# Kernel optimization log

Measured on AMD Instinct MI355X. Metric: run time of the kernel, lower is better.

Reference implementation:

```python
import jax, jax.numpy as jnp
import numpy as np

N, T, IN_F, H, C_OUT, R = 50000, 128, 6, 32, 32, 16
NUM_EDGES, N_INC = 2000, 150000


def setup_inputs() -> dict:
    key = jax.random.key(0)
    ks = jax.random.split(key, 16)
    s = 0.1  # param scale
    return {
        "price_input": jax.random.normal(ks[0], (N, T, IN_F), jnp.float32),
        "concept": jax.random.normal(ks[1], (N_INC,), jnp.float32),
        "W_ih": jax.random.normal(ks[2], (3 * H, IN_F), jnp.float32) * s,
        "W_hh": jax.random.normal(ks[3], (3 * H, H), jnp.float32) * s,
        "b_ih": jax.random.normal(ks[4], (3 * H,), jnp.float32) * s,
        "b_hh": jax.random.normal(ks[5], (3 * H,), jnp.float32) * s,
        "W1": jax.random.normal(ks[6], (C_OUT, H), jnp.float32) * s,
        "b1": jax.random.normal(ks[7], (C_OUT,), jnp.float32) * s,
        "W2": jax.random.normal(ks[8], (H, C_OUT), jnp.float32) * s,
        "b2": jax.random.normal(ks[9], (H,), jnp.float32) * s,
        "Wl": jax.random.normal(ks[10], (R, H), jnp.float32) * s,
        "bl": jax.random.normal(ks[11], (R,), jnp.float32) * s,
        "node_idx": jax.random.randint(ks[12], (N_INC,), 0, N, dtype=jnp.int32),
        "edge_idx": jax.random.randint(ks[13], (N_INC,), 0, NUM_EDGES, dtype=jnp.int32),
    }


def gru_last_hidden(x, W_ih, W_hh, b_ih, b_hh):
    # x: [N, T, IN_F] -> final hidden state [N, H] (PyTorch GRU, gate order r,z,n)
    gi_all = jnp.einsum('nti,gi->tng', x, W_ih) + b_ih  # [T, N, 3H]
    h0 = jnp.zeros((x.shape[0], W_hh.shape[1]), x.dtype)

    def step(h, gi):
        gh = h @ W_hh.T + b_hh
        ir, iz, i_n = jnp.split(gi, 3, axis=-1)
        hr, hz, h_n = jnp.split(gh, 3, axis=-1)
        r = jax.nn.sigmoid(ir + hr)
        z = jax.nn.sigmoid(iz + hz)
        n = jnp.tanh(i_n + r * h_n)
        return (1.0 - z) * n + z * h, None

    hT, _ = jax.lax.scan(step, h0, gi_all)
    return hT


def hypergraph_conv(x, W, b, node_idx, edge_idx, num_nodes, num_edges):
    # PyG HypergraphConv, use_attention=False, hyperedge_weight=1:
    # out = D^{-1} H B^{-1} H^T (X W^T) + b
    xw = x @ W.T  # [N, F_out]
    ones = jnp.ones(node_idx.shape[0], x.dtype)
    B = jax.ops.segment_sum(ones, edge_idx, num_segments=num_edges)
    Binv = jnp.where(B > 0, 1.0 / B, 0.0)
    edge_feat = jax.ops.segment_sum(xw[node_idx], edge_idx, num_segments=num_edges)
    edge_feat = edge_feat * Binv[:, None]
    D = jax.ops.segment_sum(ones, node_idx, num_segments=num_nodes)
    Dinv = jnp.where(D > 0, 1.0 / D, 0.0)
    out = jax.ops.segment_sum(edge_feat[edge_idx], node_idx, num_segments=num_nodes)
    return out * Dinv[:, None] + b


def reference(price_input, concept, W_ih, W_hh, b_ih, b_hh, W1, b1, W2, b2, Wl, bl, node_idx, edge_idx):
    # concept is only consumed on the PreAttn path (disabled here), kept for signature parity.
    num_nodes = price_input.shape[0]
    output = gru_last_hidden(price_input, W_ih, W_hh, b_ih, b_hh)  # query[0] -> [N, c_in]
    output = jax.nn.leaky_relu(output, 0.01)
    x = jax.nn.leaky_relu(
        hypergraph_conv(output, W1, b1, node_idx, edge_idx, num_nodes, NUM_EDGES), 0.2)
    x = jax.nn.leaky_relu(
        hypergraph_conv(x, W2, b2, node_idx, edge_idx, num_nodes, NUM_EDGES), 0.2)
    return jax.nn.leaky_relu(x @ Wl.T + bl, 0.01)  # [N, len(rr_num)]
```

## Files before the change

### kernel.cpp

```cpp
#include <hip/hip_runtime.h>
#include <hip/hip_bf16.h>
#include <cstdint>

#define NN 50000
#define TT 128
#define INF 6
#define HH 32
#define NE 2000
#define NI 150000
#define RR 16

typedef __attribute__((ext_vector_type(4)))  float f32x4;
typedef __attribute__((ext_vector_type(16))) float f32x16;
typedef __attribute__((ext_vector_type(8)))  short short8;

__device__ __forceinline__ float lrelu(float x, float s){ return x > 0.f ? x : s*x; }

__device__ __forceinline__ unsigned pk2(float a, float b){
  union { __hip_bfloat162 h; unsigned u; } t;
  t.h = __float22bfloat162_rn(make_float2(a, b));
  return t.u;
}
__device__ __forceinline__ void pkhl(float a, float b, unsigned &hi, unsigned &lo){
  hi = pk2(a, b);
  float ha = __uint_as_float(hi << 16);
  float hb = __uint_as_float(hi & 0xFFFF0000u);
  lo = pk2(a - ha, b - hb);
}
__device__ __forceinline__ unsigned pksplit(float x){
  unsigned h = pk2(x, 0.f) & 0xFFFFu;
  float hf = __uint_as_float(h << 16);
  unsigned l = pk2(x - hf, 0.f) & 0xFFFFu;
  return h | (l << 16);
}
__device__ __forceinline__ short8 mk8(unsigned a, unsigned b, unsigned c, unsigned d){
  union { unsigned u[4]; short8 v; } t;
  t.u[0]=a; t.u[1]=b; t.u[2]=c; t.u[3]=d;
  return t.v;
}
#define MFMA32 __builtin_amdgcn_mfma_f32_32x32x16_bf16

__global__ __launch_bounds__(64,2) void gru_mfma(
    const float* __restrict__ price,
    const float* __restrict__ W_ih, const float* __restrict__ W_hh,
    const float* __restrict__ b_ih, const float* __restrict__ b_hh,
    const float* __restrict__ W1,
    float* __restrict__ xw, float* __restrict__ eaccZ)
{
  __shared__ __align__(16) unsigned xs[2][2048];

  const int lane = threadIdx.x;
  const int a    = lane & 31;
  const int hb   = lane >> 5;
  const int n0   = blockIdx.x*32;

  { int gt = blockIdx.x*64 + lane; if (gt < NE*HH) eaccZ[gt] = 0.f; }

  for (int idx = lane; idx < 512; idx += 64){
    int bsel = idx >> 8, rem = idx & 255;
    int nd = rem >> 3, t7 = rem & 7;
    int swz = (nd&7)<<2;
    xs[bsel][nd*64 + ((t7*8+6) ^ swz)] = 0x3F803F80u;
    xs[bsel][nd*64 + ((t7*8+7) ^ swz)] = 0u;
  }

  short8 AxA[3], Ahh[3][2], Ahl[3][2];
#pragma unroll
  for (int T=0; T<3; T++){
    const int gr = T*32 + a;
    const float sc = (T<2) ? -1.44269504f : 2.88539008f;
    const float* vi = W_ih + gr*INF;
    const float w0=vi[0]*sc, w1=vi[1]*sc, w2=vi[2]*sc, w3=vi[3]*sc, w4=vi[4]*sc, w5=vi[5]*sc;
    const float bias = (b_ih[gr] + ((T<2) ? b_hh[gr] : 0.f)) * sc;
    if (hb==0) AxA[T] = mk8(pk2(w0,w1), pk2(w2,w3), pk2(w4,w5), pk2(w0,w1));
    else       AxA[T] = mk8(pk2(w2,w3), pk2(w4,w5), pksplit(bias), 0u);
#pragma unroll
    for (int m=0; m<2; m++){
      const float* wp = W_hh + gr*HH + m*16 + hb*8;
      float4 wa = *(const float4*)(wp);
      float4 wb = *(const float4*)(wp+4);
      wa.x*=sc; wa.y*=sc; wa.z*=sc; wa.w*=sc;
      wb.x*=sc; wb.y*=sc; wb.z*=sc; wb.w*=sc;
      unsigned h0,l0,h1,l1,h2,l2,h3,l3;
      pkhl(wa.x,wa.y,h0,l0); pkhl(wa.z,wa.w,h1,l1);
      pkhl(wb.x,wb.y,h2,l2); pkhl(wb.z,wb.w,h3,l3);
      Ahh[T][m] = mk8(h0,h1,h2,h3);
      Ahl[T][m] = mk8(l0,l1,l2,l3);
    }
  }
  f32x16 BHN;
#pragma unroll
  for (int r=0; r<16; r++){
    int row = (r&3) + 8*(r>>2) + 4*hb;
    BHN[r] = b_hh[2*HH + row] * 2.88539008f;
  }
  const f32x16 Z16 = {0.f,0.f,0.f,0.f,0.f,0.f,0.f,0.f,0.f,0.f,0.f,0.f,0.f,0.f,0.f,0.f};

  float h[16];
#pragma unroll
  for (int r=0;r<16;r++) h[r]=0.f;
  short8 Bh1 = mk8(0,0,0,0), Bh2 = mk8(0,0,0,0);

  float4 ld[6];
#define PREFETCH(C) { \
  _Pragma("unroll") \
  for (int q=0;q<6;q++){ \
    int id=q*64+lane, a2=id/12, off=id%12; \
    int na=n0+a2; if (na>NN-1) na=NN-1; \
    ld[q] = *(const float4*)(price + (size_t)na*(TT*INF) + (C)*48 + off*4); \
  } }
#define STAGE(BUF) { \
  _Pragma("unroll") \
  for (int q=0;q<6;q++){ \
    int id=q*64+lane, a2=id/12, off=id%12; \
    int swz=(a2&7)<<2; unsigned* row=(BUF)+a2*64; \
    _Pragma("unroll") \
    for (int p=0;p<2;p++){ \
      float e0 = p? ld[q].z : ld[q].x; \
      float e1 = p? ld[q].w : ld[q].y; \
      int b = off*4 + p*2; int ttl = b/6; int ii = b - ttl*6; \
      unsigned hi_, lo_; pkhl(e0, e1, hi_, lo_); \
      row[(ttl*8 + (ii>>1)) ^ swz]     = hi_; \
      row[(ttl*8 + 3 + (ii>>1)) ^ swz] = lo_; \
    } } }

  PREFETCH(0); STAGE(&xs[0][0]);

  const int roff = (hb<<2) ^ ((a&7)<<2);

#pragma unroll 1
  for (int c=0;c<16;c++){
    if (c<15) PREFETCH(c+1);
    const unsigned* cell = &xs[c&1][a*64];
    unsigned* sb = &xs[(c&1)^1][0];
#pragma unroll 1
    for (int tt=0; tt<8; tt++){
      union{uint4 u; short8 s;} cv;
      cv.u = *(const uint4*)(cell + ((tt*8) ^ roff));
      f32x16 aR  = MFMA32(AxA[0], cv.s, Z16, 0,0,0);
      f32x16 aZ  = MFMA32(AxA[1], cv.s, Z16, 0,0,0);
      f32x16 aNX = MFMA32(AxA[2], cv.s, Z16, 0,0,0);
      f32x16 aNH = MFMA32(Ahh[2][0], Bh1, BHN, 0,0,0);
      aR = MFMA32(Ahh[0][0], Bh1, aR, 0,0,0); aR = MFMA32(Ahh[0][1], Bh2, aR, 0,0,0);
      aR = MFMA32(Ahl[0][0], Bh1, aR, 0,0,0); aR = MFMA32(Ahl[0][1], Bh2, aR, 0,0,0);
      aZ = MFMA32(Ahh[1][0], Bh1, aZ, 0,0,0); aZ = MFMA32(Ahh[1][1], Bh2, aZ, 0,0,0);
      aZ = MFMA32(Ahl[1][0], Bh1, aZ, 0,0,0); aZ = MFMA32(Ahl[1][1], Bh2, aZ, 0,0,0);
      aNH= MFMA32(Ahh[2][1], Bh2, aNH,0,0,0);
      aNH= MFMA32(Ahl[2][0], Bh1, aNH,0,0,0); aNH= MFMA32(Ahl[2][1], Bh2, aNH,0,0,0);
#define GUPD(hvar, AR, AZ, ANX, ANH) { \
      float er = __builtin_amdgcn_exp2f(AR); \
      float rr = __builtin_amdgcn_rcpf(1.f + er); \
      float p  = (ANX) + rr*(ANH); \
      float ez = __builtin_amdgcn_exp2f(AZ); \
      float et = __builtin_amdgcn_exp2f(p); \
      float etp = et + 1.f, etm = et - 1.f; \
      float num = hvar*etp + ez*etm; \
      float den = (1.f + ez) * etp; \
      hvar = num * __builtin_amdgcn_rcpf(den); }
#pragma unroll
      for (int r=0;r<16;r++) GUPD(h[r], aR[r], aZ[r], aNX[r], aNH[r]);
      unsigned c0=pk2(h[0],h[1]),  c1=pk2(h[2],h[3]),  c2=pk2(h[4],h[5]),  c3=pk2(h[6],h[7]);
      unsigned c4=pk2(h[8],h[9]),  c5=pk2(h[10],h[11]), c6=pk2(h[12],h[13]), c7=pk2(h[14],h[15]);
      unsigned p0=__shfl_xor(c0,32,64), p1=__shfl_xor(c1,32,64);
      unsigned p2=__shfl_xor(c2,32,64), p3=__shfl_xor(c3,32,64);
      unsigned p4=__shfl_xor(c4,32,64), p5=__shfl_xor(c5,32,64);
      unsigned p6=__shfl_xor(c6,32,64), p7=__shfl_xor(c7,32,64);
      unsigned v0 = hb? p2 : c0, v1 = hb? p3 : c1, v2 = hb? c2 : p0, v3 = hb? c3 : p1;
      unsigned w0 = hb? p6 : c4, w1 = hb? p7 : c5, w2 = hb? c6 : p4, w3 = hb? c7 : p5;
      Bh1 = mk8(v0,v1,v2,v3);
      Bh2 = mk8(w0,w1,w2,w3);
    }
    if (c<15) STAGE(sb);
  }

  float* ldsF = (float*)&xs[0][0];
#pragma unroll
  for (int r=0;r<16;r++){
    int row = (r&3) + 8*(r>>2) + 4*hb;
    ldsF[a*33 + row] = lrelu(h[r], 0.01f);
  }
  float b1v[8], b2v[8];
#pragma unroll
  for (int e=0;e<8;e++){
    b1v[e] = ldsF[a*33 + hb*8 + e];
    b2v[e] = ldsF[a*33 + 16 + hb*8 + e];
  }
  unsigned q0,s0,q1,s1,q2,s2,q3,s3;
  pkhl(b1v[0],b1v[1],q0,s0); pkhl(b1v[2],b1v[3],q1,s1);
  pkhl(b1v[4],b1v[5],q2,s2); pkhl(b1v[6],b1v[7],q3,s3);
  short8 Brh1 = mk8(q0,q1,q2,q3), Brl1 = mk8(s0,s1,s2,s3);
  pkhl(b2v[0],b2v[1],q0,s0); pkhl(b2v[2],b2v[3],q1,s1);
  pkhl(b2v[4],b2v[5],q2,s2); pkhl(b2v[6],b2v[7],q3,s3);
  short8 Brh2 = mk8(q0,q1,q2,q3), Brl2 = mk8(s0,s1,s2,s3);
  short8 W1h[2], W1l[2];
#pragma unroll
  for (int m=0;m<2;m++){
    const float* wp = W1 + a*HH + m*16 + hb*8;
    float4 wa = *(const float4*)(wp);
    float4 wb = *(const float4*)(wp+4);
    unsigned h0,l0,h1,l1,h2,l2,h3,l3;
    pkhl(wa.x,wa.y,h0,l0); pkhl(wa.z,wa.w,h1,l1);
    pkhl(wb.x,wb.y,h2,l2); pkhl(wb.z,wb.w,h3,l3);
    W1h[m] = mk8(h0,h1,h2,h3);
    W1l[m] = mk8(l0,l1,l2,l3);
  }
  f32x16 o = MFMA32(W1h[0], Brh1, Z16, 0,0,0);
  o = MFMA32(W1h[1], Brh2, o, 0,0,0);
  o = MFMA32(W1h[0], Brl1, o, 0,0,0);
  o = MFMA32(W1h[1], Brl2, o, 0,0,0);
  o = MFMA32(W1l[0], Brh1, o, 0,0,0);
  o = MFMA32(W1l[1], Brh2, o, 0,0,0);
#pragma unroll
  for (int r=0;r<16;r++){
    int row = (r&3) + 8*(r>>2) + 4*hb;
    ldsF[a*33 + row] = o[r];
  }
  {
    int nn = lane>>1, f0 = (lane&1)*16;
    if (n0 + nn < NN){
#pragma unroll
      for (int q=0;q<4;q++){
        float4 v;
        v.x = ldsF[nn*33 + f0 + q*4 + 0];
        v.y = ldsF[nn*33 + f0 + q*4 + 1];
        v.z = ldsF[nn*33 + f0 + q*4 + 2];
        v.w = ldsF[nn*33 + f0 + q*4 + 3];
        *(float4*)(xw + (size_t)(n0+nn)*HH + f0 + q*4) = v;
      }
    }
  }
}

template<bool COUNT>
__global__ __launch_bounds__(256) void scat_e(const float* __restrict__ xw, const int* __restrict__ nidx,
                                              const int* __restrict__ eidx, float* __restrict__ eacc,
                                              float* __restrict__ degD, float* __restrict__ degB){
  int idx = blockIdx.x*256 + threadIdx.x;
  int i = idx >> 5, f = idx & 31;
  int nd = nidx[i], e = eidx[i];
  if (COUNT && f == 0){
    atomicAdd(&degD[nd], 1.f);
    atomicAdd(&degB[e], 1.f);
  }
  atomicAdd(&eacc[(size_t)e*HH + f], xw[(size_t)nd*HH + f]);
}
template __global__ void scat_e<true>(const float*, const int*, const int*, float*, float*, float*);
template __global__ void scat_e<false>(const float*, const int*, const int*, float*, float*, float*);

__global__ __launch_bounds__(256) void scat_n(const float* __restrict__ eacc, const float* __restrict__ degB,
                                              const int* __restrict__ nidx, const int* __restrict__ eidx,
                                              float* __restrict__ nacc){
  int idx = blockIdx.x*256 + threadIdx.x;
  int i = idx >> 5, f = idx & 31;
  int nd = nidx[i], e = eidx[i];
  float b = degB[e];
  float binv = b > 0.f ? 1.f/b : 0.f;
  atomicAdd(&nacc[(size_t)nd*HH + f], eacc[(size_t)e*HH + f]*binv);
}

__global__ __launch_bounds__(256) void finmm(float* __restrict__ nacc, const float* __restrict__ degD,
                                             const float* __restrict__ bias, const float* __restrict__ W,
                                             float* __restrict__ Y, float* __restrict__ eacc){
  __shared__ float sWt[HH*HH];
  __shared__ float sX[8*HH];
  int tid = threadIdx.x;
  if (blockIdx.x < 250) eacc[blockIdx.x*256 + tid] = 0.f;
  int f0 = tid>>5, k = tid&31;
#pragma unroll
  for (int q=0;q<4;q++) sWt[k*HH + (q*8+f0)] = W[(q*8+f0)*HH + k];
  size_t base = (size_t)blockIdx.x*8*HH;
  int n = blockIdx.x*8 + (tid>>5);
  float d = degD[n];
  float dinv = d > 0.f ? 1.f/d : 0.f;
  sX[tid] = lrelu(nacc[base + tid]*dinv + bias[tid&31], 0.2f);
  nacc[base + tid] = 0.f;
  __syncthreads();
  float a = 0.f;
#pragma unroll
  for (int kk=0;kk<HH;kk++) a += sX[(tid>>5)*HH+kk]*sWt[kk*HH+(tid&31)];
  Y[base + tid] = a;
}

__global__ __launch_bounds__(256) void fin_final(const float* __restrict__ nacc, const float* __restrict__ degD,
                                                 const float* __restrict__ b2, const float* __restrict__ Wl,
                                                 const float* __restrict__ bl, float* __restrict__ out){
  __shared__ float sWl[HH*RR];
  __shared__ float sX[8*HH];
  int tid = threadIdx.x;
#pragma unroll
  for (int q=0;q<2;q++){
    int idx = q*256 + tid;
    int r = idx >> 5, kk = idx & 31;
    sWl[kk*RR + r] = Wl[idx];
  }
  size_t base = (size_t)blockIdx.x*8*HH;
  int n = blockIdx.x*8 + (tid>>5);
  float d = degD[n];
  float dinv = d > 0.f ? 1.f/d : 0.f;
  sX[tid] = lrelu(nacc[base + tid]*dinv + b2[tid&31], 0.2f);
  __syncthreads();
  int ln = tid>>5, r = tid&31;
  if (r < RR){
    float a = bl[r];
#pragma unroll
    for (int kk=0;kk<HH;kk++) a += sX[ln*HH+kk]*sWl[kk*RR+r];
    out[(size_t)(blockIdx.x*8+ln)*RR + r] = lrelu(a, 0.01f);
  }
}

extern "C" void kernel_launch(void* const* d_in, const int* in_sizes, int n_in,
                              void* d_out, int out_size, void* d_ws, size_t ws_size,
                              hipStream_t stream){
  const float* price = (const float*)d_in[0];
  const float* W_ih = (const float*)d_in[2];
  const float* W_hh = (const float*)d_in[3];
  const float* b_ih = (const float*)d_in[4];
  const float* b_hh = (const float*)d_in[5];
  const float* W1   = (const float*)d_in[6];
  const float* b1   = (const float*)d_in[7];
  const float* W2   = (const float*)d_in[8];
  const float* b2   = (const float*)d_in[9];
  const float* Wl   = (const float*)d_in[10];
  const float* bl   = (const float*)d_in[11];
  const int* nidx   = (const int*)d_in[12];
  const int* eidx   = (const int*)d_in[13];
  float* out = (float*)d_out;

  float* ws   = (float*)d_ws;
  float* xw   = ws;
  float* nacc = ws + 1600000;
  float* degD = ws + 3200000;
  float* degB = ws + 3250000;
  float* eacc = out;

  hipMemsetAsync(nacc, 0, (1600000+52000)*sizeof(float), stream);

  gru_mfma<<<1563, 64, 0, stream>>>(price, W_ih, W_hh, b_ih, b_hh, W1, xw, eacc);

  scat_e<true><<<18750, 256, 0, stream>>>(xw, nidx, eidx, eacc, degD, degB);
  scat_n<<<18750, 256, 0, stream>>>(eacc, degB, nidx, eidx, nacc);
  finmm<<<6250, 256, 0, stream>>>(nacc, degD, b1, W2, xw, eacc);

  scat_e<false><<<18750, 256, 0, stream>>>(xw, nidx, eidx, eacc, degD, degB);
  scat_n<<<18750, 256, 0, stream>>>(eacc, degB, nidx, eidx, nacc);
  fin_final<<<6250, 256, 0, stream>>>(nacc, degD, b2, Wl, bl, out);
}
```

Baseline: 347.3 us.

## Switch GRU recurrence to 16x16x32 MFMA with 16 nodes per wave

The GRU kernel is rebuilt around 16x16x32 bf16 MFMAs. Each wave now handles 16 nodes instead of 32, and the launch doubles to 3125 blocks with launch_bounds raised to 3 waves per SIMD. The hidden state feeds back directly as the B operand, which drops the cross-half shuffles of the old 32x32 layout and halves the LDS staging buffer. The aim is to shorten the serial per-step latency chain and raise occupancy. The cost is that two lane groups in the input MFMAs carry only zero padding, and the recurrent bf16 hi/lo split now covers only the weights, since the hidden state is packed as plain bf16.

```diff
diff --git a/kernel.cpp b/kernel.cpp
--- a/kernel.cpp
+++ b/kernel.cpp
@@ -11,7 +11,6 @@
 #define RR 16
 
 typedef __attribute__((ext_vector_type(4)))  float f32x4;
-typedef __attribute__((ext_vector_type(16))) float f32x16;
 typedef __attribute__((ext_vector_type(8)))  short short8;
 
 __device__ __forceinline__ float lrelu(float x, float s){ return x > 0.f ? x : s*x; }
@@ -38,80 +37,75 @@
   t.u[0]=a; t.u[1]=b; t.u[2]=c; t.u[3]=d;
   return t.v;
 }
-#define MFMA32 __builtin_amdgcn_mfma_f32_32x32x16_bf16
-
-__global__ __launch_bounds__(64,2) void gru_mfma(
+#define MFMA16 __builtin_amdgcn_mfma_f32_16x16x32_bf16
+
+__global__ __launch_bounds__(64,3) void gru_mfma(
     const float* __restrict__ price,
     const float* __restrict__ W_ih, const float* __restrict__ W_hh,
     const float* __restrict__ b_ih, const float* __restrict__ b_hh,
     const float* __restrict__ W1,
     float* __restrict__ xw, float* __restrict__ eaccZ)
 {
-  __shared__ __align__(16) unsigned xs[2][2048];
+  __shared__ __align__(16) unsigned xs[2][1024];
 
   const int lane = threadIdx.x;
-  const int a    = lane & 31;
-  const int hb   = lane >> 5;
-  const int n0   = blockIdx.x*32;
+  const int c    = lane & 15;
+  const int g    = lane >> 4;
+  const int n0   = blockIdx.x*16;
 
   { int gt = blockIdx.x*64 + lane; if (gt < NE*HH) eaccZ[gt] = 0.f; }
 
-  for (int idx = lane; idx < 512; idx += 64){
-    int bsel = idx >> 8, rem = idx & 255;
+  for (int idx = lane; idx < 256; idx += 64){
+    int bsel = idx >> 7, rem = idx & 127;
     int nd = rem >> 3, t7 = rem & 7;
     int swz = (nd&7)<<2;
     xs[bsel][nd*64 + ((t7*8+6) ^ swz)] = 0x3F803F80u;
     xs[bsel][nd*64 + ((t7*8+7) ^ swz)] = 0u;
   }
 
-  short8 AxA[3], Ahh[3][2], Ahl[3][2];
-#pragma unroll
-  for (int T=0; T<3; T++){
-    const int gr = T*32 + a;
-    const float sc = (T<2) ? -1.44269504f : 2.88539008f;
+  short8 Ax[6], Ahh[6], Ahl[6];
+  f32x4 BHN[2];
+#pragma unroll
+  for (int q=0;q<6;q++){
+    const int gr = q*16 + c;
+    const float sc = (q<4) ? -1.44269504f : 2.88539008f;
     const float* vi = W_ih + gr*INF;
     const float w0=vi[0]*sc, w1=vi[1]*sc, w2=vi[2]*sc, w3=vi[3]*sc, w4=vi[4]*sc, w5=vi[5]*sc;
-    const float bias = (b_ih[gr] + ((T<2) ? b_hh[gr] : 0.f)) * sc;
-    if (hb==0) AxA[T] = mk8(pk2(w0,w1), pk2(w2,w3), pk2(w4,w5), pk2(w0,w1));
-    else       AxA[T] = mk8(pk2(w2,w3), pk2(w4,w5), pksplit(bias), 0u);
-#pragma unroll
-    for (int m=0; m<2; m++){
-      const float* wp = W_hh + gr*HH + m*16 + hb*8;
-      float4 wa = *(const float4*)(wp);
-      float4 wb = *(const float4*)(wp+4);
-      wa.x*=sc; wa.y*=sc; wa.z*=sc; wa.w*=sc;
-      wb.x*=sc; wb.y*=sc; wb.z*=sc; wb.w*=sc;
-      unsigned h0,l0,h1,l1,h2,l2,h3,l3;
-      pkhl(wa.x,wa.y,h0,l0); pkhl(wa.z,wa.w,h1,l1);
-      pkhl(wb.x,wb.y,h2,l2); pkhl(wb.z,wb.w,h3,l3);
-      Ahh[T][m] = mk8(h0,h1,h2,h3);
-      Ahl[T][m] = mk8(l0,l1,l2,l3);
-    }
-  }
-  f32x16 BHN;
-#pragma unroll
-  for (int r=0; r<16; r++){
-    int row = (r&3) + 8*(r>>2) + 4*hb;
-    BHN[r] = b_hh[2*HH + row] * 2.88539008f;
-  }
-  const f32x16 Z16 = {0.f,0.f,0.f,0.f,0.f,0.f,0.f,0.f,0.f,0.f,0.f,0.f,0.f,0.f,0.f,0.f};
-
-  float h[16];
-#pragma unroll
-  for (int r=0;r<16;r++) h[r]=0.f;
-  short8 Bh1 = mk8(0,0,0,0), Bh2 = mk8(0,0,0,0);
-
-  float4 ld[6];
+    const float bias = (b_ih[gr] + ((q<4) ? b_hh[gr] : 0.f)) * sc;
+    if (g==0)      Ax[q] = mk8(pk2(w0,w1), pk2(w2,w3), pk2(w4,w5), pk2(w0,w1));
+    else if (g==1) Ax[q] = mk8(pk2(w2,w3), pk2(w4,w5), pksplit(bias), 0u);
+    else           Ax[q] = mk8(0u,0u,0u,0u);
+    const float* wp = W_hh + gr*HH;
+    float4 wa = *(const float4*)(wp + 4*g);
+    float4 wb = *(const float4*)(wp + 16 + 4*g);
+    wa.x*=sc; wa.y*=sc; wa.z*=sc; wa.w*=sc;
+    wb.x*=sc; wb.y*=sc; wb.z*=sc; wb.w*=sc;
+    unsigned h0_,l0_,h1_,l1_,h2_,l2_,h3_,l3_;
+    pkhl(wa.x,wa.y,h0_,l0_); pkhl(wa.z,wa.w,h1_,l1_);
+    pkhl(wb.x,wb.y,h2_,l2_); pkhl(wb.z,wb.w,h3_,l3_);
+    Ahh[q] = mk8(h0_,h1_,h2_,h3_);
+    Ahl[q] = mk8(l0_,l1_,l2_,l3_);
+  }
+#pragma unroll
+  for (int q=0;q<2;q++)
+#pragma unroll
+    for (int j=0;j<4;j++)
+      BHN[q][j] = b_hh[2*HH + q*16 + 4*g + j] * 2.88539008f;
+  const f32x4 Z4 = {0.f,0.f,0.f,0.f};
+
+  f32x4 h0 = Z4, h1 = Z4;
+  short8 Bh = mk8(0u,0u,0u,0u);
+
+  float4 ld[3];
 #define PREFETCH(C) { \
   _Pragma("unroll") \
-  for (int q=0;q<6;q++){ \
+  for (int q=0;q<3;q++){ \
     int id=q*64+lane, a2=id/12, off=id%12; \
-    int na=n0+a2; if (na>NN-1) na=NN-1; \
-    ld[q] = *(const float4*)(price + (size_t)na*(TT*INF) + (C)*48 + off*4); \
+    ld[q] = *(const float4*)(price + (size_t)(n0+a2)*(TT*INF) + (C)*48 + off*4); \
   } }
 #define STAGE(BUF) { \
   _Pragma("unroll") \
-  for (int q=0;q<6;q++){ \
+  for (int q=0;q<3;q++){ \
     int id=q*64+lane, a2=id/12, off=id%12; \
     int swz=(a2&7)<<2; unsigned* row=(BUF)+a2*64; \
     _Pragma("unroll") \
@@ -124,29 +118,6 @@
       row[(ttl*8 + 3 + (ii>>1)) ^ swz] = lo_; \
     } } }
 
-  PREFETCH(0); STAGE(&xs[0][0]);
-
-  const int roff = (hb<<2) ^ ((a&7)<<2);
-
-#pragma unroll 1
-  for (int c=0;c<16;c++){
-    if (c<15) PREFETCH(c+1);
-    const unsigned* cell = &xs[c&1][a*64];
-    unsigned* sb = &xs[(c&1)^1][0];
-#pragma unroll 1
-    for (int tt=0; tt<8; tt++){
-      union{uint4 u; short8 s;} cv;
-      cv.u = *(const uint4*)(cell + ((tt*8) ^ roff));
-      f32x16 aR  = MFMA32(AxA[0], cv.s, Z16, 0,0,0);
-      f32x16 aZ  = MFMA32(AxA[1], cv.s, Z16, 0,0,0);
-      f32x16 aNX = MFMA32(AxA[2], cv.s, Z16, 0,0,0);
-      f32x16 aNH = MFMA32(Ahh[2][0], Bh1, BHN, 0,0,0);
-      aR = MFMA32(Ahh[0][0], Bh1, aR, 0,0,0); aR = MFMA32(Ahh[0][1], Bh2, aR, 0,0,0);
-      aR = MFMA32(Ahl[0][0], Bh1, aR, 0,0,0); aR = MFMA32(Ahl[0][1], Bh2, aR, 0,0,0);
-      aZ = MFMA32(Ahh[1][0], Bh1, aZ, 0,0,0); aZ = MFMA32(Ahh[1][1], Bh2, aZ, 0,0,0);
-      aZ = MFMA32(Ahl[1][0], Bh1, aZ, 0,0,0); aZ = MFMA32(Ahl[1][1], Bh2, aZ, 0,0,0);
-      aNH= MFMA32(Ahh[2][1], Bh2, aNH,0,0,0);
-      aNH= MFMA32(Ahl[2][0], Bh1, aNH,0,0,0); aNH= MFMA32(Ahl[2][1], Bh2, aNH,0,0,0);
 #define GUPD(hvar, AR, AZ, ANX, ANH) { \
       float er = __builtin_amdgcn_exp2f(AR); \
       float rr = __builtin_amdgcn_rcpf(1.f + er); \
@@ -157,77 +128,88 @@
       float num = hvar*etp + ez*etm; \
       float den = (1.f + ez) * etp; \
       hvar = num * __builtin_amdgcn_rcpf(den); }
-#pragma unroll
-      for (int r=0;r<16;r++) GUPD(h[r], aR[r], aZ[r], aNX[r], aNH[r]);
-      unsigned c0=pk2(h[0],h[1]),  c1=pk2(h[2],h[3]),  c2=pk2(h[4],h[5]),  c3=pk2(h[6],h[7]);
-      unsigned c4=pk2(h[8],h[9]),  c5=pk2(h[10],h[11]), c6=pk2(h[12],h[13]), c7=pk2(h[14],h[15]);
-      unsigned p0=__shfl_xor(c0,32,64), p1=__shfl_xor(c1,32,64);
-      unsigned p2=__shfl_xor(c2,32,64), p3=__shfl_xor(c3,32,64);
-      unsigned p4=__shfl_xor(c4,32,64), p5=__shfl_xor(c5,32,64);
-      unsigned p6=__shfl_xor(c6,32,64), p7=__shfl_xor(c7,32,64);
-      unsigned v0 = hb? p2 : c0, v1 = hb? p3 : c1, v2 = hb? c2 : p0, v3 = hb? c3 : p1;
-      unsigned w0 = hb? p6 : c4, w1 = hb? p7 : c5, w2 = hb? c6 : p4, w3 = hb? c7 : p5;
-      Bh1 = mk8(v0,v1,v2,v3);
-      Bh2 = mk8(w0,w1,w2,w3);
+
+  PREFETCH(0); STAGE(&xs[0][0]);
+
+  const int swzc = (c&7)<<2;
+
+#pragma unroll 1
+  for (int ch=0; ch<16; ch++){
+    if (ch<15) PREFETCH(ch+1);
+    const unsigned* cell = &xs[ch&1][c*64];
+    unsigned* sb = &xs[(ch&1)^1][0];
+#pragma unroll 1
+    for (int tt=0; tt<8; tt++){
+      union{uint4 u; short8 s;} cv;
+      cv.u.x=0u; cv.u.y=0u; cv.u.z=0u; cv.u.w=0u;
+      if (g < 2) cv.u = *(const uint4*)(cell + ((tt*8 + 4*g) ^ swzc));
+      f32x4 aR0  = MFMA16(Ax[0], cv.s, Z4, 0,0,0);
+      f32x4 aZ0  = MFMA16(Ax[2], cv.s, Z4, 0,0,0);
+      f32x4 aNX0 = MFMA16(Ax[4], cv.s, Z4, 0,0,0);
+      f32x4 aNH0 = MFMA16(Ahh[4], Bh, BHN[0], 0,0,0);
+      aR0  = MFMA16(Ahh[0], Bh, aR0, 0,0,0);
+      aR0  = MFMA16(Ahl[0], Bh, aR0, 0,0,0);
+      aZ0  = MFMA16(Ahh[2], Bh, aZ0, 0,0,0);
+      aZ0  = MFMA16(Ahl[2], Bh, aZ0, 0,0,0);
+      aNH0 = MFMA16(Ahl[4], Bh, aNH0, 0,0,0);
+#pragma unroll
+      for (int j=0;j<4;j++) GUPD(h0[j], aR0[j], aZ0[j], aNX0[j], aNH0[j]);
+      f32x4 aR1  = MFMA16(Ax[1], cv.s, Z4, 0,0,0);
+      f32x4 aZ1  = MFMA16(Ax[3], cv.s, Z4, 0,0,0);
+      f32x4 aNX1 = MFMA16(Ax[5], cv.s, Z4, 0,0,0);
+      f32x4 aNH1 = MFMA16(Ahh[5], Bh, BHN[1], 0,0,0);
+      aR1  = MFMA16(Ahh[1], Bh, aR1, 0,0,0);
+      aR1  = MFMA16(Ahl[1], Bh, aR1, 0,0,0);
+      aZ1  = MFMA16(Ahh[3], Bh, aZ1, 0,0,0);
+      aZ1  = MFMA16(Ahl[3], Bh, aZ1, 0,0,0);
+      aNH1 = MFMA16(Ahl[5], Bh, aNH1, 0,0,0);
+#pragma unroll
+      for (int j=0;j<4;j++) GUPD(h1[j], aR1[j], aZ1[j], aNX1[j], aNH1[j]);
+      Bh = mk8(pk2(h0[0],h0[1]), pk2(h0[2],h0[3]), pk2(h1[0],h1[1]), pk2(h1[2],h1[3]));
     }
-    if (c<15) STAGE(sb);
-  }
-
+    if (ch<15) STAGE(sb);
+  }
+
+  f32x4 l0, l1;
+#pragma unroll
+  for (int j=0;j<4;j++){ l0[j] = lrelu(h0[j], 0.01f); l1[j] = lrelu(h1[j], 0.01f); }
+  unsigned q0,s0,q1,s1,q2,s2,q3,s3;
+  pkhl(l0[0],l0[1],q0,s0); pkhl(l0[2],l0[3],q1,s1);
+  pkhl(l1[0],l1[1],q2,s2); pkhl(l1[2],l1[3],q3,s3);
+  short8 Brh = mk8(q0,q1,q2,q3), Brl = mk8(s0,s1,s2,s3);
+  short8 W1h[2], W1l[2];
+#pragma unroll
+  for (int q=0;q<2;q++){
+    const float* wp = W1 + (q*16 + c)*HH;
+    float4 wa = *(const float4*)(wp + 4*g);
+    float4 wb = *(const float4*)(wp + 16 + 4*g);
+    unsigned h0_,l0_,h1_,l1_,h2_,l2_,h3_,l3_;
+    pkhl(wa.x,wa.y,h0_,l0_); pkhl(wa.z,wa.w,h1_,l1_);
+    pkhl(wb.x,wb.y,h2_,l2_); pkhl(wb.z,wb.w,h3_,l3_);
+    W1h[q] = mk8(h0_,h1_,h2_,h3_);
+    W1l[q] = mk8(l0_,l1_,l2_,l3_);
+  }
+  f32x4 o0 = MFMA16(W1h[0], Brh, Z4, 0,0,0);
+  o0 = MFMA16(W1l[0], Brh, o0, 0,0,0);
+  o0 = MFMA16(W1h[0], Brl, o0, 0,0,0);
+  f32x4 o1 = MFMA16(W1h[1], Brh, Z4, 0,0,0);
+  o1 = MFMA16(W1l[1], Brh, o1, 0,0,0);
+  o1 = MFMA16(W1h[1], Brl, o1, 0,0,0);
   float* ldsF = (float*)&xs[0][0];
 #pragma unroll
-  for (int r=0;r<16;r++){
-    int row = (r&3) + 8*(r>>2) + 4*hb;
-    ldsF[a*33 + row] = lrelu(h[r], 0.01f);
-  }
-  float b1v[8], b2v[8];
-#pragma unroll
-  for (int e=0;e<8;e++){
-    b1v[e] = ldsF[a*33 + hb*8 + e];
-    b2v[e] = ldsF[a*33 + 16 + hb*8 + e];
-  }
-  unsigned q0,s0,q1,s1,q2,s2,q3,s3;
-  pkhl(b1v[0],b1v[1],q0,s0); pkhl(b1v[2],b1v[3],q1,s1);
-  pkhl(b1v[4],b1v[5],q2,s2); pkhl(b1v[6],b1v[7],q3,s3);
-  short8 Brh1 = mk8(q0,q1,q2,q3), Brl1 = mk8(s0,s1,s2,s3);
-  pkhl(b2v[0],b2v[1],q0,s0); pkhl(b2v[2],b2v[3],q1,s1);
-  pkhl(b2v[4],b2v[5],q2,s2); pkhl(b2v[6],b2v[7],q3,s3);
-  short8 Brh2 = mk8(q0,q1,q2,q3), Brl2 = mk8(s0,s1,s2,s3);
-  short8 W1h[2], W1l[2];
-#pragma unroll
-  for (int m=0;m<2;m++){
-    const float* wp = W1 + a*HH + m*16 + hb*8;
-    float4 wa = *(const float4*)(wp);
-    float4 wb = *(const float4*)(wp+4);
-    unsigned h0,l0,h1,l1,h2,l2,h3,l3;
-    pkhl(wa.x,wa.y,h0,l0); pkhl(wa.z,wa.w,h1,l1);
-    pkhl(wb.x,wb.y,h2,l2); pkhl(wb.z,wb.w,h3,l3);
-    W1h[m] = mk8(h0,h1,h2,h3);
-    W1l[m] = mk8(l0,l1,l2,l3);
-  }
-  f32x16 o = MFMA32(W1h[0], Brh1, Z16, 0,0,0);
-  o = MFMA32(W1h[1], Brh2, o, 0,0,0);
-  o = MFMA32(W1h[0], Brl1, o, 0,0,0);
-  o = MFMA32(W1h[1], Brl2, o, 0,0,0);
-  o = MFMA32(W1l[0], Brh1, o, 0,0,0);
-  o = MFMA32(W1l[1], Brh2, o, 0,0,0);
-#pragma unroll
-  for (int r=0;r<16;r++){
-    int row = (r&3) + 8*(r>>2) + 4*hb;
-    ldsF[a*33 + row] = o[r];
+  for (int j=0;j<4;j++){
+    ldsF[c*33 + 4*g + j]      = o0[j];
+    ldsF[c*33 + 16 + 4*g + j] = o1[j];
   }
   {
-    int nn = lane>>1, f0 = (lane&1)*16;
-    if (n0 + nn < NN){
-#pragma unroll
-      for (int q=0;q<4;q++){
-        float4 v;
-        v.x = ldsF[nn*33 + f0 + q*4 + 0];
-        v.y = ldsF[nn*33 + f0 + q*4 + 1];
-        v.z = ldsF[nn*33 + f0 + q*4 + 2];
-        v.w = ldsF[nn*33 + f0 + q*4 + 3];
-        *(float4*)(xw + (size_t)(n0+nn)*HH + f0 + q*4) = v;
-      }
-    }
+    int nn = lane>>2, f0 = (lane&3)*8;
+    float4 v0, v1;
+    v0.x = ldsF[nn*33 + f0 + 0]; v0.y = ldsF[nn*33 + f0 + 1];
+    v0.z = ldsF[nn*33 + f0 + 2]; v0.w = ldsF[nn*33 + f0 + 3];
+    v1.x = ldsF[nn*33 + f0 + 4]; v1.y = ldsF[nn*33 + f0 + 5];
+    v1.z = ldsF[nn*33 + f0 + 6]; v1.w = ldsF[nn*33 + f0 + 7];
+    *(float4*)(xw + (size_t)(n0+nn)*HH + f0)     = v0;
+    *(float4*)(xw + (size_t)(n0+nn)*HH + f0 + 4) = v1;
   }
 }
 
@@ -335,7 +317,7 @@
 
   hipMemsetAsync(nacc, 0, (1600000+52000)*sizeof(float), stream);
 
-  gru_mfma<<<1563, 64, 0, stream>>>(price, W_ih, W_hh, b_ih, b_hh, W1, xw, eacc);
+  gru_mfma<<<3125, 64, 0, stream>>>(price, W_ih, W_hh, b_ih, b_hh, W1, xw, eacc);
 
   scat_e<true><<<18750, 256, 0, stream>>>(xw, nidx, eidx, eacc, degD, degB);
   scat_n<<<18750, 256, 0, stream>>>(eacc, degB, nidx, eidx, nacc);
```

Measured after the change: 355.9 us. +2.5%, slower.

## Replace atomic scatter hypergraph aggregation with CSR-based gather kernels

Applied to the files above, without the earlier changes.

Builds CSR incidence lists per edge and per node (count, single-block scan, fill) and replaces the atomic scatter-add kernels with wavefront-per-segment gather reductions that write results directly. This removes heavy float atomic contention on the edge and node accumulators and the memset of the node accumulator. It adds three small preprocessing kernels, including a serial single-block scan, and stores the CSR arrays in the output buffer as scratch. Summation order is no longer atomic-order dependent.

```diff
diff --git a/kernel.cpp b/kernel.cpp
--- a/kernel.cpp
+++ b/kernel.cpp
@@ -231,31 +231,93 @@
   }
 }
 
-template<bool COUNT>
-__global__ __launch_bounds__(256) void scat_e(const float* __restrict__ xw, const int* __restrict__ nidx,
-                                              const int* __restrict__ eidx, float* __restrict__ eacc,
-                                              float* __restrict__ degD, float* __restrict__ degB){
-  int idx = blockIdx.x*256 + threadIdx.x;
-  int i = idx >> 5, f = idx & 31;
-  int nd = nidx[i], e = eidx[i];
-  if (COUNT && f == 0){
-    atomicAdd(&degD[nd], 1.f);
-    atomicAdd(&degB[e], 1.f);
-  }
-  atomicAdd(&eacc[(size_t)e*HH + f], xw[(size_t)nd*HH + f]);
-}
-template __global__ void scat_e<true>(const float*, const int*, const int*, float*, float*, float*);
-template __global__ void scat_e<false>(const float*, const int*, const int*, float*, float*, float*);
-
-__global__ __launch_bounds__(256) void scat_n(const float* __restrict__ eacc, const float* __restrict__ degB,
-                                              const int* __restrict__ nidx, const int* __restrict__ eidx,
-                                              float* __restrict__ nacc){
-  int idx = blockIdx.x*256 + threadIdx.x;
-  int i = idx >> 5, f = idx & 31;
-  int nd = nidx[i], e = eidx[i];
-  float b = degB[e];
-  float binv = b > 0.f ? 1.f/b : 0.f;
-  atomicAdd(&nacc[(size_t)nd*HH + f], eacc[(size_t)e*HH + f]*binv);
+#define O_EACC  0
+#define O_EOFF  64000
+#define O_NOFF  66001
+#define O_ECUR  116002
+#define O_NCUR  118002
+#define O_ELIST 168002
+#define O_NLIST 318002
+
+__global__ __launch_bounds__(256) void csr_count(const int* __restrict__ nidx, const int* __restrict__ eidx,
+                                                 int* __restrict__ ncnt, int* __restrict__ ecnt){
+  int i = blockIdx.x*256 + threadIdx.x;
+  if (i < NI){
+    atomicAdd(&ecnt[eidx[i]], 1);
+    atomicAdd(&ncnt[nidx[i]], 1);
+  }
+}
+
+__global__ __launch_bounds__(1024) void csr_scan(int* __restrict__ ncntcur, int* __restrict__ noff,
+                                                 int* __restrict__ ecntcur, int* __restrict__ eoff){
+  __shared__ int lds[1024];
+  int tid = threadIdx.x;
+  {
+    const int N = NN, C = 49;
+    int base = tid*C, s = 0;
+    for (int k=0;k<C;k++){ int i=base+k; if (i<N) s += ncntcur[i]; }
+    lds[tid] = s; __syncthreads();
+    if (tid==0){ int run=0; for (int t=0;t<1024;t++){ int v=lds[t]; lds[t]=run; run+=v; } }
+    __syncthreads();
+    int run = lds[tid];
+    for (int k=0;k<C;k++){ int i=base+k; if (i<N){ int cv=ncntcur[i]; noff[i]=run; ncntcur[i]=run; run+=cv; } }
+    if (tid==0) noff[N] = NI;
+    __syncthreads();
+  }
+  {
+    const int N = NE, C = 2;
+    int base = tid*C, s = 0;
+    for (int k=0;k<C;k++){ int i=base+k; if (i<N) s += ecntcur[i]; }
+    lds[tid] = s; __syncthreads();
+    if (tid==0){ int run=0; for (int t=0;t<1024;t++){ int v=lds[t]; lds[t]=run; run+=v; } }
+    __syncthreads();
+    int run = lds[tid];
+    for (int k=0;k<C;k++){ int i=base+k; if (i<N){ int cv=ecntcur[i]; eoff[i]=run; ecntcur[i]=run; run+=cv; } }
+    if (tid==0) eoff[N] = NI;
+  }
+}
+
+__global__ __launch_bounds__(256) void csr_fill(const int* __restrict__ nidx, const int* __restrict__ eidx,
+                                                int* __restrict__ ncur, int* __restrict__ ecur,
+                                                int* __restrict__ nlist, int* __restrict__ elist){
+  int i = blockIdx.x*256 + threadIdx.x;
+  if (i < NI){
+    int nd = nidx[i], e = eidx[i];
+    int se = atomicAdd(&ecur[e], 1);
+    elist[se] = nd;
+    int sn = atomicAdd(&ncur[nd], 1);
+    nlist[sn] = e;
+  }
+}
+
+__global__ __launch_bounds__(256) void egather(const float* __restrict__ xw, const int* __restrict__ elist,
+                                               const int* __restrict__ eoff, float* __restrict__ eacc){
+  int wv = blockIdx.x*4 + (threadIdx.x>>6);
+  int lane = threadIdx.x & 63;
+  int f = lane & 31, k = lane >> 5;
+  int o0 = eoff[wv], o1 = eoff[wv+1];
+  float acc = 0.f;
+  for (int j = o0 + k; j < o1; j += 2)
+    acc += xw[(size_t)elist[j]*HH + f];
+  acc += __shfl_xor(acc, 32, 64);
+  int d = o1 - o0;
+  float bi = d > 0 ? 1.f/(float)d : 0.f;
+  if (lane < 32) eacc[(size_t)wv*HH + lane] = acc*bi;
+}
+
+__global__ __launch_bounds__(256) void ngather(const float* __restrict__ eacc, const int* __restrict__ nlist,
+                                               const int* __restrict__ noff, float* __restrict__ nacc,
+                                               float* __restrict__ degD){
+  int wv = blockIdx.x*4 + (threadIdx.x>>6);
+  int lane = threadIdx.x & 63;
+  int f = lane & 31, k = lane >> 5;
+  int o0 = noff[wv], o1 = noff[wv+1];
+  float acc = 0.f;
+  for (int j = o0 + k; j < o1; j += 2)
+    acc += eacc[(size_t)nlist[j]*HH + f];
+  acc += __shfl_xor(acc, 32, 64);
+  if (lane == 0) degD[wv] = (float)(o1 - o0);
+  if (lane < 32) nacc[(size_t)wv*HH + lane] = acc;
 }
 
 __global__ __launch_bounds__(256) void finmm(float* __restrict__ nacc, const float* __restrict__ degD,
@@ -325,23 +387,34 @@
   const int* nidx   = (const int*)d_in[12];
   const int* eidx   = (const int*)d_in[13];
   float* out = (float*)d_out;
+  int*  outI = (int*)d_out;
 
   float* ws   = (float*)d_ws;
   float* xw   = ws;
   float* nacc = ws + 1600000;
   float* degD = ws + 3200000;
-  float* degB = ws + 3250000;
-  float* eacc = out;
-
-  hipMemsetAsync(nacc, 0, (1600000+52000)*sizeof(float), stream);
+
+  float* eacc = out  + O_EACC;
+  int* eoff   = outI + O_EOFF;
+  int* noff   = outI + O_NOFF;
+  int* ecur   = outI + O_ECUR;
+  int* ncur   = outI + O_NCUR;
+  int* elist  = outI + O_ELIST;
+  int* nlist  = outI + O_NLIST;
+
+  hipMemsetAsync(ecur, 0, (O_ELIST - O_ECUR)*sizeof(int), stream);
+
+  csr_count<<<586, 256, 0, stream>>>(nidx, eidx, ncur, ecur);
+  csr_scan<<<1, 1024, 0, stream>>>(ncur, noff, ecur, eoff);
+  csr_fill<<<586, 256, 0, stream>>>(nidx, eidx, ncur, ecur, nlist, elist);
 
   gru_mfma<<<1563, 64, 0, stream>>>(price, W_ih, W_hh, b_ih, b_hh, W1, xw, eacc);
 
-  scat_e<true><<<18750, 256, 0, stream>>>(xw, nidx, eidx, eacc, degD, degB);
-  scat_n<<<18750, 256, 0, stream>>>(eacc, degB, nidx, eidx, nacc);
+  egather<<<500,  256, 0, stream>>>(xw, elist, eoff, eacc);
+  ngather<<<12500,256, 0, stream>>>(eacc, nlist, noff, nacc, degD);
   finmm<<<6250, 256, 0, stream>>>(nacc, degD, b1, W2, xw, eacc);
 
-  scat_e<false><<<18750, 256, 0, stream>>>(xw, nidx, eidx, eacc, degD, degB);
-  scat_n<<<18750, 256, 0, stream>>>(eacc, degB, nidx, eidx, nacc);
+  egather<<<500,  256, 0, stream>>>(xw, elist, eoff, eacc);
+  ngather<<<12500,256, 0, stream>>>(eacc, nlist, noff, nacc, degD);
   fin_final<<<6250, 256, 0, stream>>>(nacc, degD, b2, Wl, bl, out);
 }
```

Measured after the change: 514.2 us. +48.1%, slower.

## Interleave two independent node tiles per wave in GRU recurrence

Applied to the files above, without the earlier changes.

Each GRU wave now advances two independent 32-node tiles in lockstep, with separate hidden states, MFMA chains and LDS staging buffers. Interleaving the two tiles' matrix-multiply chains and gate updates gives the scheduler independent work to hide MFMA and transcendental latency inside the serial time recurrence. The grid is halved and launch bounds relaxed to one wave per block-slot, so more registers are available. The trade-off is fewer resident waves, which may leave some SIMDs underused, plus higher register and LDS use per wave.

```diff
diff --git a/kernel.cpp b/kernel.cpp
--- a/kernel.cpp
+++ b/kernel.cpp
@@ -40,28 +40,29 @@
 }
 #define MFMA32 __builtin_amdgcn_mfma_f32_32x32x16_bf16
 
-__global__ __launch_bounds__(64,2) void gru_mfma(
+__global__ __launch_bounds__(64,1) void gru_mfma(
     const float* __restrict__ price,
     const float* __restrict__ W_ih, const float* __restrict__ W_hh,
     const float* __restrict__ b_ih, const float* __restrict__ b_hh,
     const float* __restrict__ W1,
     float* __restrict__ xw, float* __restrict__ eaccZ)
 {
-  __shared__ __align__(16) unsigned xs[2][2048];
+  __shared__ __align__(16) unsigned xs[2][2][2048];
 
   const int lane = threadIdx.x;
   const int a    = lane & 31;
   const int hb   = lane >> 5;
-  const int n0   = blockIdx.x*32;
-
-  { int gt = blockIdx.x*64 + lane; if (gt < NE*HH) eaccZ[gt] = 0.f; }
-
-  for (int idx = lane; idx < 512; idx += 64){
-    int bsel = idx >> 8, rem = idx & 255;
+  const int n0A  = blockIdx.x*64;
+  const int n0B  = n0A + 32;
+
+  for (int gt = blockIdx.x*64 + lane; gt < NE*HH; gt += 782*64) eaccZ[gt] = 0.f;
+
+  for (int idx = lane; idx < 1024; idx += 64){
+    int t = idx >> 9, bsel = (idx >> 8) & 1, rem = idx & 255;
     int nd = rem >> 3, t7 = rem & 7;
     int swz = (nd&7)<<2;
-    xs[bsel][nd*64 + ((t7*8+6) ^ swz)] = 0x3F803F80u;
-    xs[bsel][nd*64 + ((t7*8+7) ^ swz)] = 0u;
+    xs[t][bsel][nd*64 + ((t7*8+6) ^ swz)] = 0x3F803F80u;
+    xs[t][bsel][nd*64 + ((t7*8+7) ^ swz)] = 0u;
   }
 
   short8 AxA[3], Ahh[3][2], Ahl[3][2];
@@ -96,57 +97,35 @@
   }
   const f32x16 Z16 = {0.f,0.f,0.f,0.f,0.f,0.f,0.f,0.f,0.f,0.f,0.f,0.f,0.f,0.f,0.f,0.f};
 
-  float h[16];
-#pragma unroll
-  for (int r=0;r<16;r++) h[r]=0.f;
-  short8 Bh1 = mk8(0,0,0,0), Bh2 = mk8(0,0,0,0);
-
-  float4 ld[6];
-#define PREFETCH(C) { \
+  float hA[16], hB[16];
+#pragma unroll
+  for (int r=0;r<16;r++){ hA[r]=0.f; hB[r]=0.f; }
+  short8 Bh1A = mk8(0,0,0,0), Bh2A = mk8(0,0,0,0);
+  short8 Bh1B = mk8(0,0,0,0), Bh2B = mk8(0,0,0,0);
+
+  float4 ldA[6], ldB[6];
+#define PREFETCH(LD, N0, C) { \
   _Pragma("unroll") \
   for (int q=0;q<6;q++){ \
     int id=q*64+lane, a2=id/12, off=id%12; \
-    int na=n0+a2; if (na>NN-1) na=NN-1; \
-    ld[q] = *(const float4*)(price + (size_t)na*(TT*INF) + (C)*48 + off*4); \
+    int na=(N0)+a2; if (na>NN-1) na=NN-1; \
+    LD[q] = *(const float4*)(price + (size_t)na*(TT*INF) + (C)*48 + off*4); \
   } }
-#define STAGE(BUF) { \
+#define STAGE(LD, BUF) { \
   _Pragma("unroll") \
   for (int q=0;q<6;q++){ \
     int id=q*64+lane, a2=id/12, off=id%12; \
     int swz=(a2&7)<<2; unsigned* row=(BUF)+a2*64; \
     _Pragma("unroll") \
     for (int p=0;p<2;p++){ \
-      float e0 = p? ld[q].z : ld[q].x; \
-      float e1 = p? ld[q].w : ld[q].y; \
+      float e0 = p? LD[q].z : LD[q].x; \
+      float e1 = p? LD[q].w : LD[q].y; \
       int b = off*4 + p*2; int ttl = b/6; int ii = b - ttl*6; \
       unsigned hi_, lo_; pkhl(e0, e1, hi_, lo_); \
       row[(ttl*8 + (ii>>1)) ^ swz]     = hi_; \
       row[(ttl*8 + 3 + (ii>>1)) ^ swz] = lo_; \
     } } }
 
-  PREFETCH(0); STAGE(&xs[0][0]);
-
-  const int roff = (hb<<2) ^ ((a&7)<<2);
-
-#pragma unroll 1
-  for (int c=0;c<16;c++){
-    if (c<15) PREFETCH(c+1);
-    const unsigned* cell = &xs[c&1][a*64];
-    unsigned* sb = &xs[(c&1)^1][0];
-#pragma unroll 1
-    for (int tt=0; tt<8; tt++){
-      union{uint4 u; short8 s;} cv;
-      cv.u = *(const uint4*)(cell + ((tt*8) ^ roff));
-      f32x16 aR  = MFMA32(AxA[0], cv.s, Z16, 0,0,0);
-      f32x16 aZ  = MFMA32(AxA[1], cv.s, Z16, 0,0,0);
-      f32x16 aNX = MFMA32(AxA[2], cv.s, Z16, 0,0,0);
-      f32x16 aNH = MFMA32(Ahh[2][0], Bh1, BHN, 0,0,0);
-      aR = MFMA32(Ahh[0][0], Bh1, aR, 0,0,0); aR = MFMA32(Ahh[0][1], Bh2, aR, 0,0,0);
-      aR = MFMA32(Ahl[0][0], Bh1, aR, 0,0,0); aR = MFMA32(Ahl[0][1], Bh2, aR, 0,0,0);
-      aZ = MFMA32(Ahh[1][0], Bh1, aZ, 0,0,0); aZ = MFMA32(Ahh[1][1], Bh2, aZ, 0,0,0);
-      aZ = MFMA32(Ahl[1][0], Bh1, aZ, 0,0,0); aZ = MFMA32(Ahl[1][1], Bh2, aZ, 0,0,0);
-      aNH= MFMA32(Ahh[2][1], Bh2, aNH,0,0,0);
-      aNH= MFMA32(Ahl[2][0], Bh1, aNH,0,0,0); aNH= MFMA32(Ahl[2][1], Bh2, aNH,0,0,0);
 #define GUPD(hvar, AR, AZ, ANX, ANH) { \
       float er = __builtin_amdgcn_exp2f(AR); \
       float rr = __builtin_amdgcn_rcpf(1.f + er); \
@@ -157,41 +136,61 @@
       float num = hvar*etp + ez*etm; \
       float den = (1.f + ez) * etp; \
       hvar = num * __builtin_amdgcn_rcpf(den); }
-#pragma unroll
-      for (int r=0;r<16;r++) GUPD(h[r], aR[r], aZ[r], aNX[r], aNH[r]);
-      unsigned c0=pk2(h[0],h[1]),  c1=pk2(h[2],h[3]),  c2=pk2(h[4],h[5]),  c3=pk2(h[6],h[7]);
-      unsigned c4=pk2(h[8],h[9]),  c5=pk2(h[10],h[11]), c6=pk2(h[12],h[13]), c7=pk2(h[14],h[15]);
-      unsigned p0=__shfl_xor(c0,32,64), p1=__shfl_xor(c1,32,64);
-      unsigned p2=__shfl_xor(c2,32,64), p3=__shfl_xor(c3,32,64);
-      unsigned p4=__shfl_xor(c4,32,64), p5=__shfl_xor(c5,32,64);
-      unsigned p6=__shfl_xor(c6,32,64), p7=__shfl_xor(c7,32,64);
-      unsigned v0 = hb? p2 : c0, v1 = hb? p3 : c1, v2 = hb? c2 : p0, v3 = hb? c3 : p1;
-      unsigned w0 = hb? p6 : c4, w1 = hb? p7 : c5, w2 = hb? c6 : p4, w3 = hb? c7 : p5;
-      Bh1 = mk8(v0,v1,v2,v3);
-      Bh2 = mk8(w0,w1,w2,w3);
+
+#define MCHAIN(CV, B1, B2, AR, AZ, ANX, ANH) { \
+      AR  = MFMA32(AxA[0], CV, Z16, 0,0,0); \
+      AZ  = MFMA32(AxA[1], CV, Z16, 0,0,0); \
+      ANX = MFMA32(AxA[2], CV, Z16, 0,0,0); \
+      ANH = MFMA32(Ahh[2][0], B1, BHN, 0,0,0); \
+      AR = MFMA32(Ahh[0][0], B1, AR, 0,0,0); AR = MFMA32(Ahh[0][1], B2, AR, 0,0,0); \
+      AR = MFMA32(Ahl[0][0], B1, AR, 0,0,0); AR = MFMA32(Ahl[0][1], B2, AR, 0,0,0); \
+      AZ = MFMA32(Ahh[1][0], B1, AZ, 0,0,0); AZ = MFMA32(Ahh[1][1], B2, AZ, 0,0,0); \
+      AZ = MFMA32(Ahl[1][0], B1, AZ, 0,0,0); AZ = MFMA32(Ahl[1][1], B2, AZ, 0,0,0); \
+      ANH= MFMA32(Ahh[2][1], B2, ANH,0,0,0); \
+      ANH= MFMA32(Ahl[2][0], B1, ANH,0,0,0); ANH= MFMA32(Ahl[2][1], B2, ANH,0,0,0); }
+
+#define PACKB(H, B1, B2) { \
+      unsigned c0=pk2(H[0],H[1]),  c1=pk2(H[2],H[3]),  c2=pk2(H[4],H[5]),  c3=pk2(H[6],H[7]); \
+      unsigned c4=pk2(H[8],H[9]),  c5=pk2(H[10],H[11]), c6=pk2(H[12],H[13]), c7=pk2(H[14],H[15]); \
+      unsigned p0=__shfl_xor(c0,32,64), p1=__shfl_xor(c1,32,64); \
+      unsigned p2=__shfl_xor(c2,32,64), p3=__shfl_xor(c3,32,64); \
+      unsigned p4=__shfl_xor(c4,32,64), p5=__shfl_xor(c5,32,64); \
+      unsigned p6=__shfl_xor(c6,32,64), p7=__shfl_xor(c7,32,64); \
+      unsigned v0 = hb? p2 : c0, v1 = hb? p3 : c1, v2 = hb? c2 : p0, v3 = hb? c3 : p1; \
+      unsigned w0 = hb? p6 : c4, w1 = hb? p7 : c5, w2 = hb? c6 : p4, w3 = hb? c7 : p5; \
+      B1 = mk8(v0,v1,v2,v3); \
+      B2 = mk8(w0,w1,w2,w3); }
+
+  PREFETCH(ldA, n0A, 0); PREFETCH(ldB, n0B, 0);
+  STAGE(ldA, &xs[0][0][0]); STAGE(ldB, &xs[1][0][0]);
+
+  const int roff = (hb<<2) ^ ((a&7)<<2);
+
+#pragma unroll 1
+  for (int c=0;c<16;c++){
+    if (c<15){ PREFETCH(ldA, n0A, c+1); PREFETCH(ldB, n0B, c+1); }
+    const unsigned* cellA = &xs[0][c&1][a*64];
+    const unsigned* cellB = &xs[1][c&1][a*64];
+    unsigned* sbA = &xs[0][(c&1)^1][0];
+    unsigned* sbB = &xs[1][(c&1)^1][0];
+#pragma unroll 1
+    for (int tt=0; tt<8; tt++){
+      union{uint4 u; short8 s;} cvA, cvB;
+      cvA.u = *(const uint4*)(cellA + ((tt*8) ^ roff));
+      cvB.u = *(const uint4*)(cellB + ((tt*8) ^ roff));
+      f32x16 aR, aZ, aNX, aNH, bR, bZ, bNX, bNH;
+      MCHAIN(cvA.s, Bh1A, Bh2A, aR, aZ, aNX, aNH);
+      MCHAIN(cvB.s, Bh1B, Bh2B, bR, bZ, bNX, bNH);
+#pragma unroll
+      for (int r=0;r<16;r++) GUPD(hA[r], aR[r], aZ[r], aNX[r], aNH[r]);
+      PACKB(hA, Bh1A, Bh2A);
+#pragma unroll
+      for (int r=0;r<16;r++) GUPD(hB[r], bR[r], bZ[r], bNX[r], bNH[r]);
+      PACKB(hB, Bh1B, Bh2B);
     }
-    if (c<15) STAGE(sb);
-  }
-
-  float* ldsF = (float*)&xs[0][0];
-#pragma unroll
-  for (int r=0;r<16;r++){
-    int row = (r&3) + 8*(r>>2) + 4*hb;
-    ldsF[a*33 + row] = lrelu(h[r], 0.01f);
-  }
-  float b1v[8], b2v[8];
-#pragma unroll
-  for (int e=0;e<8;e++){
-    b1v[e] = ldsF[a*33 + hb*8 + e];
-    b2v[e] = ldsF[a*33 + 16 + hb*8 + e];
-  }
-  unsigned q0,s0,q1,s1,q2,s2,q3,s3;
-  pkhl(b1v[0],b1v[1],q0,s0); pkhl(b1v[2],b1v[3],q1,s1);
-  pkhl(b1v[4],b1v[5],q2,s2); pkhl(b1v[6],b1v[7],q3,s3);
-  short8 Brh1 = mk8(q0,q1,q2,q3), Brl1 = mk8(s0,s1,s2,s3);
-  pkhl(b2v[0],b2v[1],q0,s0); pkhl(b2v[2],b2v[3],q1,s1);
-  pkhl(b2v[4],b2v[5],q2,s2); pkhl(b2v[6],b2v[7],q3,s3);
-  short8 Brh2 = mk8(q0,q1,q2,q3), Brl2 = mk8(s0,s1,s2,s3);
+    if (c<15){ STAGE(ldA, sbA); STAGE(ldB, sbB); }
+  }
+
   short8 W1h[2], W1l[2];
 #pragma unroll
   for (int m=0;m<2;m++){
@@ -204,31 +203,56 @@
     W1h[m] = mk8(h0,h1,h2,h3);
     W1l[m] = mk8(l0,l1,l2,l3);
   }
-  f32x16 o = MFMA32(W1h[0], Brh1, Z16, 0,0,0);
-  o = MFMA32(W1h[1], Brh2, o, 0,0,0);
-  o = MFMA32(W1h[0], Brl1, o, 0,0,0);
-  o = MFMA32(W1h[1], Brl2, o, 0,0,0);
-  o = MFMA32(W1l[0], Brh1, o, 0,0,0);
-  o = MFMA32(W1l[1], Brh2, o, 0,0,0);
-#pragma unroll
-  for (int r=0;r<16;r++){
-    int row = (r&3) + 8*(r>>2) + 4*hb;
-    ldsF[a*33 + row] = o[r];
-  }
-  {
-    int nn = lane>>1, f0 = (lane&1)*16;
-    if (n0 + nn < NN){
-#pragma unroll
-      for (int q=0;q<4;q++){
-        float4 v;
-        v.x = ldsF[nn*33 + f0 + q*4 + 0];
-        v.y = ldsF[nn*33 + f0 + q*4 + 1];
-        v.z = ldsF[nn*33 + f0 + q*4 + 2];
-        v.w = ldsF[nn*33 + f0 + q*4 + 3];
-        *(float4*)(xw + (size_t)(n0+nn)*HH + f0 + q*4) = v;
-      }
-    }
-  }
+
+#define EPILOG(H, LDSF, N0) { \
+  _Pragma("unroll") \
+  for (int r=0;r<16;r++){ \
+    int row = (r&3) + 8*(r>>2) + 4*hb; \
+    (LDSF)[a*33 + row] = lrelu(H[r], 0.01f); \
+  } \
+  float b1v[8], b2v[8]; \
+  _Pragma("unroll") \
+  for (int e=0;e<8;e++){ \
+    b1v[e] = (LDSF)[a*33 + hb*8 + e]; \
+    b2v[e] = (LDSF)[a*33 + 16 + hb*8 + e]; \
+  } \
+  unsigned q0,s0,q1,s1,q2,s2,q3,s3; \
+  pkhl(b1v[0],b1v[1],q0,s0); pkhl(b1v[2],b1v[3],q1,s1); \
+  pkhl(b1v[4],b1v[5],q2,s2); pkhl(b1v[6],b1v[7],q3,s3); \
+  short8 Brh1 = mk8(q0,q1,q2,q3), Brl1 = mk8(s0,s1,s2,s3); \
+  pkhl(b2v[0],b2v[1],q0,s0); pkhl(b2v[2],b2v[3],q1,s1); \
+  pkhl(b2v[4],b2v[5],q2,s2); pkhl(b2v[6],b2v[7],q3,s3); \
+  short8 Brh2 = mk8(q0,q1,q2,q3), Brl2 = mk8(s0,s1,s2,s3); \
+  f32x16 o = MFMA32(W1h[0], Brh1, Z16, 0,0,0); \
+  o = MFMA32(W1h[1], Brh2, o, 0,0,0); \
+  o = MFMA32(W1h[0], Brl1, o, 0,0,0); \
+  o = MFMA32(W1h[1], Brl2, o, 0,0,0); \
+  o = MFMA32(W1l[0], Brh1, o, 0,0,0); \
+  o = MFMA32(W1l[1], Brh2, o, 0,0,0); \
+  _Pragma("unroll") \
+  for (int r=0;r<16;r++){ \
+    int row = (r&3) + 8*(r>>2) + 4*hb; \
+    (LDSF)[a*33 + row] = o[r]; \
+  } \
+  { \
+    int nn = lane>>1, f0 = (lane&1)*16; \
+    if ((N0) + nn < NN){ \
+      _Pragma("unroll") \
+      for (int q=0;q<4;q++){ \
+        float4 v; \
+        v.x = (LDSF)[nn*33 + f0 + q*4 + 0]; \
+        v.y = (LDSF)[nn*33 + f0 + q*4 + 1]; \
+        v.z = (LDSF)[nn*33 + f0 + q*4 + 2]; \
+        v.w = (LDSF)[nn*33 + f0 + q*4 + 3]; \
+        *(float4*)(xw + (size_t)((N0)+nn)*HH + f0 + q*4) = v; \
+      } \
+    } \
+  } }
+
+  float* ldsFA = (float*)&xs[0][0][0];
+  float* ldsFB = (float*)&xs[1][0][0];
+  EPILOG(hA, ldsFA, n0A);
+  EPILOG(hB, ldsFB, n0B);
 }
 
 template<bool COUNT>
@@ -335,7 +359,7 @@
 
   hipMemsetAsync(nacc, 0, (1600000+52000)*sizeof(float), stream);
 
-  gru_mfma<<<1563, 64, 0, stream>>>(price, W_ih, W_hh, b_ih, b_hh, W1, xw, eacc);
+  gru_mfma<<<782, 64, 0, stream>>>(price, W_ih, W_hh, b_ih, b_hh, W1, xw, eacc);
 
   scat_e<true><<<18750, 256, 0, stream>>>(xw, nidx, eidx, eacc, degD, degB);
   scat_n<<<18750, 256, 0, stream>>>(eacc, degB, nidx, eidx, nacc);
```

Result: slower. 401.9 us (+15.7%).
